# Kernel optimization log

Measured on AMD Instinct MI355X. Metric: run time of the kernel, lower is better.

## Reference

```python
import jax, jax.numpy as jnp
import numpy as np

B, N, N_FEAT = 16, 1024, 128
N_LAYER, AGG_HIDDEN, FC_HIDDEN, N_CLASS = 3, 64, 128, 10
NEG_INF = -9e15
LEAKY_SLOPE = 0.2


def setup_inputs() -> dict:
    key = jax.random.key(0)
    ks = jax.random.split(key, 8)
    x = jax.random.normal(ks[0], (B, N, N_FEAT), dtype=jnp.float32)
    adj = jax.random.randint(ks[1], (B, N, N), 0, 2).astype(jnp.float32)
    # per-layer GAT params, stacked over layers
    Ws = jax.random.normal(ks[2], (N_LAYER, N_FEAT, AGG_HIDDEN), dtype=jnp.float32) * 0.1
    a1 = jax.random.normal(ks[3], (N_LAYER, AGG_HIDDEN), dtype=jnp.float32) * 0.1
    a2 = jax.random.normal(ks[4], (N_LAYER, AGG_HIDDEN), dtype=jnp.float32) * 0.1
    W1 = jax.random.normal(ks[5], (AGG_HIDDEN * N_LAYER, FC_HIDDEN), dtype=jnp.float32) * 0.05
    b1 = jnp.zeros((FC_HIDDEN,), dtype=jnp.float32)
    W2 = jax.random.normal(ks[6], (FC_HIDDEN, N_CLASS), dtype=jnp.float32) * 0.05
    b2 = jnp.zeros((N_CLASS,), dtype=jnp.float32)
    return {"x": x, "adj": adj, "Ws": Ws, "a1": a1, "a2": a2,
            "W1": W1, "b1": b1, "W2": W2, "b2": b2}


def _gat_layer(x, adj, W, a1, a2):
    # h: [B, N, H]
    h = jnp.einsum('bnf,fh->bnh', x, W)
    # e_ij = LeakyReLU(a1.h_i + a2.h_j)  -- split-a trick, avoids [B,N,N,2H]
    f1 = jnp.einsum('bnh,h->bn', h, a1)
    f2 = jnp.einsum('bnh,h->bn', h, a2)
    e = jax.nn.leaky_relu(f1[:, :, None] + f2[:, None, :], LEAKY_SLOPE)  # [B,N,N]
    att = jax.nn.softmax(jnp.where(adj > 0, e, NEG_INF), axis=-1)
    return jnp.einsum('bnm,bmh->bnh', att, h)


def reference(x, adj, Ws, a1, a2, W1, b1, W2, b2):
    # eval mode: dropout is identity
    outs = [jax.nn.relu(_gat_layer(x, adj, Ws[i], a1[i], a2[i]))
            for i in range(N_LAYER)]
    h = jnp.concatenate(outs, axis=2)          # [B, N, H*L]
    pooled = jnp.mean(h, axis=1)               # 'avg' pool over nodes -> [B, H*L]
    z = jax.nn.relu(pooled @ W1 + b1)
    return jax.nn.softmax(z @ W2 + b2, axis=-1)  # [B, n_class]
```

## Files before the change

kernel.cpp:

```cpp
#include <hip/hip_runtime.h>

#define B 16
#define N 1024
#define NF 128
#define NL 3
#define AH 64
#define HC 192
#define FCH 128
#define NC 10
#define L2E 1.44269504088896f

typedef __attribute__((ext_vector_type(8))) short bf16x8;
typedef __attribute__((ext_vector_type(4))) float f32x4;
typedef __attribute__((ext_vector_type(4))) unsigned int u32x4;

static __device__ __forceinline__ unsigned short f2bf(float f) {
  unsigned int x = __builtin_bit_cast(unsigned int, f);
  return (unsigned short)((x + 0x7fffu + ((x >> 16) & 1u)) >> 16);
}
static __device__ __forceinline__ float bf2f(unsigned short u) {
  unsigned int x = ((unsigned int)u) << 16;
  return __builtin_bit_cast(float, x);
}

__global__ __launch_bounds__(256, 2) void k_feat(
    const float* __restrict__ x, const float* __restrict__ Ws,
    const float* __restrict__ a1, const float* __restrict__ a2,
    unsigned short* __restrict__ h_f, float* __restrict__ f1g,
    float* __restrict__ f2g, float* __restrict__ pooled)
{
  __shared__ float xs[64][132];
  __shared__ unsigned short wl[2][64][136];
  unsigned short (*hlds)[72] = (unsigned short(*)[72])&xs[0][0];
  const int t = threadIdx.x;
  const int n0g = blockIdx.x * 64;
  const int gb = n0g >> 10, nl0 = n0g & 1023;
  const int wv = t >> 6, lane = t & 63;
  const int lr = lane & 15, lg = lane >> 4;
  const int lrow = wv * 16 + lr;
  const int wcol = t & 63, woct = t >> 6;

  if (blockIdx.x == 0) {
    #pragma unroll
    for (int i = 0; i < 12; ++i) pooled[i * 256 + t] = 0.f;
  }

#define LOADW(R, L) {                                                         \
    _Pragma("unroll")                                                         \
    for (int p = 0; p < 4; ++p) {                                             \
      const int oct = p * 4 + woct;                                           \
      _Pragma("unroll")                                                       \
      for (int i = 0; i < 8; ++i)                                             \
        R[p][i] = Ws[((size_t)(L) * NF + oct * 8 + i) * AH + wcol];           \
    } }
#define WRITEW(R) {                                                           \
    _Pragma("unroll")                                                         \
    for (int p = 0; p < 4; ++p) {                                             \
      const int oct = p * 4 + woct;                                           \
      bf16x8 hv, lv;                                                          \
      _Pragma("unroll")                                                       \
      for (int i = 0; i < 8; ++i) {                                           \
        const unsigned short hi = f2bf(R[p][i]);                              \
        hv[i] = (short)hi;                                                    \
        lv[i] = (short)f2bf(R[p][i] - bf2f(hi));                              \
      }                                                                       \
      *(bf16x8*)&wl[0][wcol][oct * 8] = hv;                                   \
      *(bf16x8*)&wl[1][wcol][oct * 8] = lv;                                   \
    } }
#define MFMAL(L) {                                                            \
    _Pragma("unroll")                                                         \
    for (int n2 = 0; n2 < 4; ++n2) {                                          \
      const int n = (L) * 4 + n2;                                             \
      _Pragma("unroll")                                                       \
      for (int kf = 0; kf < 4; ++kf) {                                        \
        const bf16x8 whi = *(const bf16x8*)&wl[0][n2 * 16 + lr][kf * 32 + lg * 8]; \
        const bf16x8 wlo = *(const bf16x8*)&wl[1][n2 * 16 + lr][kf * 32 + lg * 8]; \
        acc[n] = __builtin_amdgcn_mfma_f32_16x16x32_bf16(xhi[kf], whi, acc[n], 0, 0, 0); \
        acc[n] = __builtin_amdgcn_mfma_f32_16x16x32_bf16(xhi[kf], wlo, acc[n], 0, 0, 0); \
        acc[n] = __builtin_amdgcn_mfma_f32_16x16x32_bf16(xlo[kf], whi, acc[n], 0, 0, 0); \
      }                                                                       \
    } }

  float wrA[4][8], wrB[4][8];
  LOADW(wrA, 0);

  #pragma unroll
  for (int p = 0; p < 8; ++p) {
    const int q = p * 256 + t;
    const int row = q >> 5, c4 = (q & 31) * 4;
    *(float4*)&xs[row][c4] = *(const float4*)&x[(size_t)(n0g + row) * NF + c4];
  }
  __syncthreads();

  bf16x8 xhi[4], xlo[4];
  #pragma unroll
  for (int kf = 0; kf < 4; ++kf) {
    const float4 q0 = *(const float4*)&xs[lrow][kf * 32 + lg * 8];
    const float4 q1 = *(const float4*)&xs[lrow][kf * 32 + lg * 8 + 4];
    const float xv[8] = {q0.x, q0.y, q0.z, q0.w, q1.x, q1.y, q1.z, q1.w};
    #pragma unroll
    for (int e = 0; e < 8; ++e) {
      const unsigned short hi = f2bf(xv[e]);
      xhi[kf][e] = (short)hi;
      xlo[kf][e] = (short)f2bf(xv[e] - bf2f(hi));
    }
  }

  f32x4 acc[12];
  #pragma unroll
  for (int n = 0; n < 12; ++n) acc[n] = (f32x4){0.f, 0.f, 0.f, 0.f};

  WRITEW(wrA);
  LOADW(wrB, 1);
  __syncthreads();
  MFMAL(0);
  __syncthreads();
  WRITEW(wrB);
  LOADW(wrA, 2);
  __syncthreads();
  MFMAL(1);
  __syncthreads();
  WRITEW(wrA);
  __syncthreads();
  MFMAL(2);

#undef LOADW
#undef WRITEW
#undef MFMAL

  float s1[3][4], s2[3][4];
  #pragma unroll
  for (int l = 0; l < 3; ++l)
    #pragma unroll
    for (int r = 0; r < 4; ++r) { s1[l][r] = 0.f; s2[l][r] = 0.f; }
  #pragma unroll
  for (int n = 0; n < 12; ++n) {
    const int col = n * 16 + lr;
    const float a1v = a1[col] * L2E, a2v = a2[col] * L2E;
    const int l = n >> 2;
    #pragma unroll
    for (int r = 0; r < 4; ++r) {
      s1[l][r] += acc[n][r] * a1v;
      s2[l][r] += acc[n][r] * a2v;
    }
  }
  #pragma unroll
  for (int off = 1; off < 16; off <<= 1)
    #pragma unroll
    for (int l = 0; l < 3; ++l)
      #pragma unroll
      for (int r = 0; r < 4; ++r) {
        s1[l][r] += __shfl_xor(s1[l][r], off);
        s2[l][r] += __shfl_xor(s2[l][r], off);
      }
  if (lr == 0) {
    #pragma unroll
    for (int l = 0; l < 3; ++l)
      #pragma unroll
      for (int r = 0; r < 4; ++r) {
        const int rw = n0g + wv * 16 + lg * 4 + r;
        f1g[(size_t)l * (B * N) + rw] = s1[l][r];
        f2g[(size_t)l * (B * N) + rw] = s2[l][r];
      }
  }

  __syncthreads();
  #pragma unroll
  for (int n = 0; n < 12; ++n) {
    const int col = n * 16 + lr;
    #pragma unroll
    for (int rp = 0; rp < 2; ++rp) {
      const unsigned int pr = (unsigned int)f2bf(acc[n][rp * 2]) |
                              ((unsigned int)f2bf(acc[n][rp * 2 + 1]) << 16);
      *(unsigned int*)&hlds[col][wv * 16 + lg * 4 + rp * 2] = pr;
    }
  }
  __syncthreads();
  #pragma unroll
  for (int p = 0; p < 6; ++p) {
    const int widx = p * 256 + t;
    const int lane_w = widx & 63;
    const int jb2 = (widx >> 6) & 1;
    const int n_w = (widx >> 7) & 3;
    const int l_w = widx >> 9;
    const int col = l_w * 64 + n_w * 16 + (lane_w & 15);
    const int jloc = jb2 * 32 + (lane_w >> 4) * 8;
    const size_t off =
        ((((size_t)(gb * 3 + l_w) * 4 + n_w) * 32 + (nl0 >> 5) + jb2) * 64 + lane_w) * 8;
    *(uint4*)&h_f[off] = *(const uint4*)&hlds[col][jloc];
  }
}

__global__ __launch_bounds__(256) void k_tab(
    const float* __restrict__ f1, const float* __restrict__ f2,
    float* __restrict__ tab)
{
  __shared__ float red[4];
  const int lb = blockIdx.x, t = threadIdx.x;
  const float* f2p = f2 + (size_t)lb * N;
  const float* f1p = f1 + (size_t)lb * N;

  float v = -1e30f;
  #pragma unroll
  for (int i = 0; i < 4; ++i) v = fmaxf(v, f2p[i * 256 + t]);
  #pragma unroll
  for (int off = 32; off; off >>= 1) v = fmaxf(v, __shfl_down(v, off));
  if ((t & 63) == 0) red[t >> 6] = v;
  __syncthreads();
  const float mx = fmaxf(fmaxf(red[0], red[1]), fmaxf(red[2], red[3]));

  #pragma unroll
  for (int i = 0; i < 4; ++i) {
    const int j = i * 256 + t;
    const float q2 = f2p[j];
    const float q1 = f1p[j];
    const float tt = q1 + mx;
    const float sr = fmaxf(tt, 0.f) + 0.2f * fminf(tt, 0.f);
    tab[(size_t)(0 * NL * B + lb) * N + j] = exp2f(q2);
    tab[(size_t)(1 * NL * B + lb) * N + j] = exp2f(0.2f * q2);
    tab[(size_t)(2 * NL * B + lb) * N + j] = exp2f(q1 - sr);
    tab[(size_t)(3 * NL * B + lb) * N + j] = exp2f(0.2f * q1 - sr);
  }
}

__global__ __launch_bounds__(192) void k_att(
    const float* __restrict__ adj, const unsigned short* __restrict__ h_f,
    const float* __restrict__ tab, float* __restrict__ pooled)
{
  const int bid = blockIdx.x;
  const int blk = (bid & 7) * 128 + (bid >> 3);
  const int b = blk >> 6;
  const int i0 = (blk & 63) * 16;
  const int t = threadIdx.x;
  const int l = t >> 6, lane = t & 63;
  const int lr = lane & 15, lg = lane >> 4;
  const int msh = (lg & 1) * 8;

  __shared__ unsigned short sm[16][66];

  const float* ap = adj + ((size_t)(b * N + i0)) * N;
  for (int q = t; q < 1024; q += 192) {
    const int row = q >> 6, ch = q & 63;
    const float* p = ap + (size_t)row * N + ch * 16;
    unsigned int bits = 0;
    #pragma unroll
    for (int qq = 0; qq < 4; ++qq) {
      const uint4 u = *(const uint4*)(p + qq * 4);
      bits |= (u.x ? 1u : 0u) << (qq * 4 + 0);
      bits |= (u.y ? 1u : 0u) << (qq * 4 + 1);
      bits |= (u.z ? 1u : 0u) << (qq * 4 + 2);
      bits |= (u.w ? 1u : 0u) << (qq * 4 + 3);
    }
    sm[row][ch] = (unsigned short)bits;
  }

  const int lb = l * B + b;
  const float* ut = tab + (size_t)(0 * NL * B + lb) * N;
  const float* vt = tab + (size_t)(1 * NL * B + lb) * N;
  const float A = tab[(size_t)(2 * NL * B + lb) * N + i0 + lr];
  const float C = tab[(size_t)(3 * NL * B + lb) * N + i0 + lr];

  const unsigned short* hfb = h_f + ((size_t)(b * 3 + l)) * 65536;
  const bf16x8 ones = {(short)0x3F80, (short)0x3F80, (short)0x3F80, (short)0x3F80,
                       (short)0x3F80, (short)0x3F80, (short)0x3F80, (short)0x3F80};

  f32x4 acc[4];
  #pragma unroll
  for (int n = 0; n < 4; ++n) acc[n] = (f32x4){0.f, 0.f, 0.f, 0.f};
  f32x4 accd = (f32x4){0.f, 0.f, 0.f, 0.f};

  __syncthreads();

#define LOADJ(BUF, MW, J) {                                                   \
    const int jj = (J) & (N - 1);                                             \
    const int jt = jj >> 6;                                                   \
    const unsigned int s0 = sm[lr][jt * 4 + (lg >> 1)];                       \
    const unsigned int s1 = sm[lr][jt * 4 + 2 + (lg >> 1)];                   \
    MW = ((s0 >> msh) & 0xffu) | (((s1 >> msh) & 0xffu) << 8);                \
    _Pragma("unroll")                                                         \
    for (int q = 0; q < 8; ++q) {                                             \
      const int ks = q >> 2, n = q & 3;                                       \
      BUF[q] = *(const bf16x8*)&hfb[(((size_t)n * 32 + (jj >> 5) + ks) * 64 + \
                                     lane) * 8];                              \
    } }

#define COMPJ(BUF, MW, J) {                                                   \
    _Pragma("unroll")                                                         \
    for (int ks = 0; ks < 2; ++ks) {                                          \
      const int kb = ((J) & (N - 1)) + ks * 32 + lg * 8;                      \
      const float4 u0 = *(const float4*)&ut[kb];                              \
      const float4 u1 = *(const float4*)&ut[kb + 4];                          \
      const float4 v0 = *(const float4*)&vt[kb];                              \
      const float4 v1 = *(const float4*)&vt[kb + 4];                          \
      const unsigned int mby = ((MW) >> (ks * 8)) & 0xffu;                    \
      const float uu[8] = {u0.x, u0.y, u0.z, u0.w, u1.x, u1.y, u1.z, u1.w};   \
      const float vv[8] = {v0.x, v0.y, v0.z, v0.w, v1.x, v1.y, v1.z, v1.w};   \
      unsigned int pk[4];                                                     \
      _Pragma("unroll")                                                       \
      for (int ep = 0; ep < 4; ++ep) {                                        \
        unsigned int pr[2];                                                   \
        _Pragma("unroll")                                                     \
        for (int h = 0; h < 2; ++h) {                                         \
          const int e = ep * 2 + h;                                           \
                  \
          const float p = fmaxf(A * uu[e], C * vv[e]);                        \
          const unsigned int sel =                                            \
              (unsigned int)(((int)(mby << (31 - e))) >> 31);                 \
          pr[h] = (__builtin_bit_cast(unsigned int, p) + 0x8000u) & sel;      \
        }                                                                     \
        pk[ep] = __builtin_amdgcn_perm(pr[1], pr[0], 0x07060302u);            \
      }                                                                       \
      const u32x4 pkv = {pk[0], pk[1], pk[2], pk[3]};                         \
      const bf16x8 av = __builtin_bit_cast(bf16x8, pkv);                      \
      _Pragma("unroll")                                                       \
      for (int n = 0; n < 4; ++n)                                             \
        acc[n] = __builtin_amdgcn_mfma_f32_16x16x32_bf16(av, BUF[ks * 4 + n], \
                                                         acc[n], 0, 0, 0);    \
      accd = __builtin_amdgcn_mfma_f32_16x16x32_bf16(av, ones, accd, 0, 0, 0);\
    } }

#define SBAR __builtin_amdgcn_sched_barrier(0)

  bf16x8 bA[8], bB[8];
  unsigned int mwA, mwB;
  LOADJ(bA, mwA, 0);
  SBAR;
  for (int j0 = 0; j0 < N; j0 += 128) {
    LOADJ(bB, mwB, j0 + 64);
    SBAR;
    COMPJ(bA, mwA, j0);
    SBAR;
    LOADJ(bA, mwA, j0 + 128);
    SBAR;
    COMPJ(bB, mwB, j0 + 64);
    SBAR;
  }
#undef LOADJ
#undef COMPJ
#undef SBAR

  float dn[4];
  #pragma unroll
  for (int r = 0; r < 4; ++r) dn[r] = 1.f / fmaxf(accd[r], 1e-37f);

  #pragma unroll
  for (int n = 0; n < 4; ++n) {
    float csum = 0.f;
    #pragma unroll
    for (int r = 0; r < 4; ++r) csum += fmaxf(acc[n][r] * dn[r], 0.f);
    csum += __shfl_xor(csum, 16);
    csum += __shfl_xor(csum, 32);
    if (lg == 0) atomicAdd(&pooled[b * HC + l * 64 + n * 16 + lr], csum);
  }
}

__global__ __launch_bounds__(192) void k_head(
    const float* __restrict__ pooled_sums, const float* __restrict__ W1,
    const float* __restrict__ b1, const float* __restrict__ W2,
    const float* __restrict__ b2, float* __restrict__ out)
{
  const int b = blockIdx.x, t = threadIdx.x;
  __shared__ float pooled[HC];
  __shared__ float z[FCH];
  __shared__ float logits[NC];

  if (t < HC) pooled[t] = pooled_sums[b * HC + t] * (1.f / (float)N);
  __syncthreads();

  if (t < FCH) {
    float a = b1[t];
    #pragma unroll 4
    for (int f = 0; f < HC; ++f) a += pooled[f] * W1[(size_t)f * FCH + t];
    z[t] = a > 0.f ? a : 0.f;
  }
  __syncthreads();

  if (t < NC) {
    float a = b2[t];
    #pragma unroll 4
    for (int f = 0; f < FCH; ++f) a += z[f] * W2[(size_t)f * NC + t];
    logits[t] = a;
  }
  __syncthreads();

  if (t == 0) {
    float mxl = logits[0];
    for (int c = 1; c < NC; ++c) mxl = fmaxf(mxl, logits[c]);
    float e[NC], sum = 0.f;
    for (int c = 0; c < NC; ++c) { e[c] = __expf(logits[c] - mxl); sum += e[c]; }
    const float inv = 1.f / sum;
    for (int c = 0; c < NC; ++c) out[b * NC + c] = e[c] * inv;
  }
}

extern "C" void kernel_launch(void* const* d_in, const int* in_sizes, int n_in,
                              void* d_out, int out_size, void* d_ws, size_t ws_size,
                              hipStream_t stream)
{
  const float* x   = (const float*)d_in[0];
  const float* adj = (const float*)d_in[1];
  const float* Ws  = (const float*)d_in[2];
  const float* a1  = (const float*)d_in[3];
  const float* a2  = (const float*)d_in[4];
  const float* W1  = (const float*)d_in[5];
  const float* b1  = (const float*)d_in[6];
  const float* W2  = (const float*)d_in[7];
  const float* b2  = (const float*)d_in[8];
  float* out = (float*)d_out;

  unsigned short* h_f   = (unsigned short*)d_ws;
  float*          f1    = (float*)(h_f + (size_t)B * HC * N);
  float*          f2    = f1 + (size_t)NL * B * N;
  float*          pooled= f2 + (size_t)NL * B * N;
  float*          tab   = pooled + B * HC + 16;

  k_feat<<<256, 256, 0, stream>>>(x, Ws, a1, a2, h_f, f1, f2, pooled);
  k_tab <<<NL * B, 256, 0, stream>>>(f1, f2, tab);
  k_att <<<1024, 192, 0, stream>>>(adj, h_f, tab, pooled);
  k_head<<<B, 192, 0, stream>>>(pooled, W1, b1, W2, b2, out);
}
```

Baseline: 82.37 us.

## Split attention blocks per layer and stage packed bf16 u/v table in LDS

The attention kernel now launches one 64-thread block per (batch, row-stripe, layer) instead of one 192-thread block covering all three layers, so each block repacks the adjacency bits itself. The exp tables u and v are packed as two bf16 values per 32-bit word and copied into shared memory, so the inner loop reads them from LDS instead of global memory. This cuts table bandwidth and increases block-level parallelism. The cost is that each 16-row adjacency stripe is now read and bit-packed three times, and u/v carry reduced precision.

New measurement: 74.89 us. 9.1% less time.

```diff
diff --git a/kernel.cpp b/kernel.cpp
--- a/kernel.cpp
+++ b/kernel.cpp
@@ -193,7 +193,8 @@
 
 __global__ __launch_bounds__(256) void k_tab(
     const float* __restrict__ f1, const float* __restrict__ f2,
-    float* __restrict__ tab)
+    unsigned int* __restrict__ tabuv, float* __restrict__ tabA,
+    float* __restrict__ tabC)
 {
   __shared__ float red[4];
   const int lb = blockIdx.x, t = threadIdx.x;
@@ -216,32 +217,35 @@
     const float q1 = f1p[j];
     const float tt = q1 + mx;
     const float sr = fmaxf(tt, 0.f) + 0.2f * fminf(tt, 0.f);
-    tab[(size_t)(0 * NL * B + lb) * N + j] = exp2f(q2);
-    tab[(size_t)(1 * NL * B + lb) * N + j] = exp2f(0.2f * q2);
-    tab[(size_t)(2 * NL * B + lb) * N + j] = exp2f(q1 - sr);
-    tab[(size_t)(3 * NL * B + lb) * N + j] = exp2f(0.2f * q1 - sr);
-  }
-}
-
-__global__ __launch_bounds__(192) void k_att(
+    tabuv[(size_t)lb * N + j] =
+        (unsigned int)f2bf(exp2f(q2)) | ((unsigned int)f2bf(exp2f(0.2f * q2)) << 16);
+    tabA[(size_t)lb * N + j] = exp2f(q1 - sr);
+    tabC[(size_t)lb * N + j] = exp2f(0.2f * q1 - sr);
+  }
+}
+
+__global__ __launch_bounds__(64) void k_att(
     const float* __restrict__ adj, const unsigned short* __restrict__ h_f,
-    const float* __restrict__ tab, float* __restrict__ pooled)
+    const unsigned int* __restrict__ tabuv, const float* __restrict__ tabA,
+    const float* __restrict__ tabC, float* __restrict__ pooled)
 {
   const int bid = blockIdx.x;
-  const int blk = (bid & 7) * 128 + (bid >> 3);
-  const int b = blk >> 6;
-  const int i0 = (blk & 63) * 16;
-  const int t = threadIdx.x;
-  const int l = t >> 6, lane = t & 63;
+  const int idx = (bid & 7) * 384 + (bid >> 3);
+  const int stripe = idx / 3;
+  const int l = idx - stripe * 3;
+  const int b = stripe >> 6;
+  const int i0 = (stripe & 63) * 16;
+  const int lane = threadIdx.x;
   const int lr = lane & 15, lg = lane >> 4;
   const int msh = (lg & 1) * 8;
 
   __shared__ unsigned short sm[16][66];
+  __shared__ unsigned int uvp[N];
 
   const float* ap = adj + ((size_t)(b * N + i0)) * N;
-  for (int q = t; q < 1024; q += 192) {
-    const int row = q >> 6, ch = q & 63;
-    const float* p = ap + (size_t)row * N + ch * 16;
+  #pragma unroll 4
+  for (int i = 0; i < 16; ++i) {
+    const float* p = ap + (size_t)i * N + lane * 16;
     unsigned int bits = 0;
     #pragma unroll
     for (int qq = 0; qq < 4; ++qq) {
@@ -251,14 +255,17 @@
       bits |= (u.z ? 1u : 0u) << (qq * 4 + 2);
       bits |= (u.w ? 1u : 0u) << (qq * 4 + 3);
     }
-    sm[row][ch] = (unsigned short)bits;
+    sm[i][lane] = (unsigned short)bits;
   }
 
   const int lb = l * B + b;
-  const float* ut = tab + (size_t)(0 * NL * B + lb) * N;
-  const float* vt = tab + (size_t)(1 * NL * B + lb) * N;
-  const float A = tab[(size_t)(2 * NL * B + lb) * N + i0 + lr];
-  const float C = tab[(size_t)(3 * NL * B + lb) * N + i0 + lr];
+  #pragma unroll
+  for (int i = 0; i < 4; ++i)
+    *(uint4*)&uvp[i * 256 + lane * 4] =
+        *(const uint4*)&tabuv[(size_t)lb * N + i * 256 + lane * 4];
+
+  const float A = tabA[(size_t)lb * N + i0 + lr];
+  const float C = tabC[(size_t)lb * N + i0 + lr];
 
   const unsigned short* hfb = h_f + ((size_t)(b * 3 + l)) * 65536;
   const bf16x8 ones = {(short)0x3F80, (short)0x3F80, (short)0x3F80, (short)0x3F80,
@@ -288,13 +295,11 @@
     _Pragma("unroll")                                                         \
     for (int ks = 0; ks < 2; ++ks) {                                          \
       const int kb = ((J) & (N - 1)) + ks * 32 + lg * 8;                      \
-      const float4 u0 = *(const float4*)&ut[kb];                              \
-      const float4 u1 = *(const float4*)&ut[kb + 4];                          \
-      const float4 v0 = *(const float4*)&vt[kb];                              \
-      const float4 v1 = *(const float4*)&vt[kb + 4];                          \
+      const uint4 w0 = *(const uint4*)&uvp[kb];                               \
+      const uint4 w1 = *(const uint4*)&uvp[kb + 4];                           \
+      const unsigned int wk[8] = {w0.x, w0.y, w0.z, w0.w,                     \
+                                  w1.x, w1.y, w1.z, w1.w};                    \
       const unsigned int mby = ((MW) >> (ks * 8)) & 0xffu;                    \
-      const float uu[8] = {u0.x, u0.y, u0.z, u0.w, u1.x, u1.y, u1.z, u1.w};   \
-      const float vv[8] = {v0.x, v0.y, v0.z, v0.w, v1.x, v1.y, v1.z, v1.w};   \
       unsigned int pk[4];                                                     \
       _Pragma("unroll")                                                       \
       for (int ep = 0; ep < 4; ++ep) {                                        \
@@ -302,8 +307,10 @@
         _Pragma("unroll")                                                     \
         for (int h = 0; h < 2; ++h) {                                         \
           const int e = ep * 2 + h;                                           \
+          const float ue = __builtin_bit_cast(float, wk[e] << 16);            \
+          const float ve = __builtin_bit_cast(float, wk[e] & 0xffff0000u);    \
                   \
-          const float p = fmaxf(A * uu[e], C * vv[e]);                        \
+          const float p = fmaxf(A * ue, C * ve);                              \
           const unsigned int sel =                                            \
               (unsigned int)(((int)(mby << (31 - e))) >> 31);                 \
           pr[h] = (__builtin_bit_cast(unsigned int, p) + 0x8000u) & sel;      \
@@ -412,10 +419,12 @@
   float*          f1    = (float*)(h_f + (size_t)B * HC * N);
   float*          f2    = f1 + (size_t)NL * B * N;
   float*          pooled= f2 + (size_t)NL * B * N;
-  float*          tab   = pooled + B * HC + 16;
+  unsigned int*   tabuv = (unsigned int*)(pooled + B * HC + 16);
+  float*          tabA  = (float*)(tabuv + (size_t)NL * B * N);
+  float*          tabC  = tabA + (size_t)NL * B * N;
 
   k_feat<<<256, 256, 0, stream>>>(x, Ws, a1, a2, h_f, f1, f2, pooled);
-  k_tab <<<NL * B, 256, 0, stream>>>(f1, f2, tab);
-  k_att <<<1024, 192, 0, stream>>>(adj, h_f, tab, pooled);
+  k_tab <<<NL * B, 256, 0, stream>>>(f1, f2, tabuv, tabA, tabC);
+  k_att <<<3072, 64, 0, stream>>>(adj, h_f, tabuv, tabA, tabC, pooled);
   k_head<<<B, 192, 0, stream>>>(pooled, W1, b1, W2, b2, out);
 }
```
